# Kernel optimization log

Measured on AMD Instinct MI355X. Metric: run time of the kernel, lower is better.

The kernel has to match this reference:

```python
import jax, jax.numpy as jnp
import numpy as np

N_NODES = 50000
N_EDGES = 400000
IN_DIM = 128
HIDDEN = 128
OUT_DIM = 128
MIX = 4

def _gelu(x):
    return jax.nn.gelu(x, approximate=False)  # torch default erf-GELU

def setup_inputs() -> dict:
    key = jax.random.key(0)
    ks = jax.random.split(key, 8)
    X = jax.random.normal(ks[0], (N_NODES, IN_DIM), dtype=jnp.float32)
    edge_index = jax.random.randint(ks[1], (2, N_EDGES), 0, N_NODES, dtype=jnp.int64)
    s = lambda fan_in: 1.0 / np.sqrt(fan_in)
    W1 = jax.random.uniform(ks[2], (HIDDEN, IN_DIM), jnp.float32, -s(IN_DIM), s(IN_DIM))
    b1 = jax.random.uniform(ks[3], (HIDDEN,), jnp.float32, -s(IN_DIM), s(IN_DIM))
    WA = jax.random.uniform(ks[4], (HIDDEN, HIDDEN), jnp.float32, -s(HIDDEN), s(HIDDEN))
    WB = jax.random.uniform(ks[5], (MIX, HIDDEN), jnp.float32, -s(HIDDEN), s(HIDDEN))
    W2 = jax.random.uniform(ks[6], (OUT_DIM, 2 * HIDDEN), jnp.float32, -s(2 * HIDDEN), s(2 * HIDDEN))
    b2 = jax.random.uniform(ks[7], (OUT_DIM,), jnp.float32, -s(2 * HIDDEN), s(2 * HIDDEN))
    return {"X": X, "edge_index": edge_index, "W1": W1, "b1": b1,
            "WA": WA, "WB": WB, "W2": W2, "b2": b2}

def reference(X, edge_index, W1, b1, WA, WB, W2, b2):
    num_nodes = X.shape[0]
    # ff1 -> gelu (dropout identity in eval)
    H = _gelu(X @ W1.T + b1)                       # (N, h)
    src, dst = edge_index[0], edge_index[1]
    X_src = H[src]                                 # (E, h) gather
    # hyper target weights per edge
    W_tar = _gelu(X_src @ WA.T) @ WB.T             # (E, m)
    # per-edge outer product, scatter_add over dst
    cross = X_src[:, :, None] * W_tar[:, None, :]  # (E, h, m)
    agg = jax.ops.segment_sum(cross, dst, num_segments=num_nodes)  # (N, h, m)
    agg = _gelu(agg)
    # gather back per edge, contract mix dim
    out_edge = jnp.einsum('ehm,em->eh', agg[dst], W_tar)  # (E, h)
    # scatter_mean over dst
    ones = jnp.ones((src.shape[0],), X.dtype)
    cnt = jax.ops.segment_sum(ones, dst, num_segments=num_nodes)   # (N,)
    agg_node = jax.ops.segment_sum(out_edge, dst, num_segments=num_nodes)
    agg_node = agg_node / jnp.maximum(cnt, 1.0)[:, None]           # (N, h)
    # root connection + gelu, ff2
    feat = _gelu(jnp.concatenate([agg_node, H], axis=1))           # (N, 2h)
    out = feat @ W2.T + b2                                          # (N, out)
    return out
```

## Files before the change

kernel.cpp:

```cpp
#include <hip/hip_runtime.h>
#include <hip/hip_bf16.h>

#define NN 50000
#define NE 400000
#define NT 3125

typedef unsigned short u16;
typedef short short8 __attribute__((ext_vector_type(8)));
typedef float f32x4 __attribute__((ext_vector_type(4)));

__device__ __forceinline__ float geluf(float x){ return 0.5f*x*(1.0f+erff(x*0.70710678118654752440f)); }
__device__ __forceinline__ u16 f2bfb(float f){
  union { __hip_bfloat16 h; u16 u; } cv; cv.h = __float2bfloat16(f); return cv.u;
}
__device__ __forceinline__ float bfb2f(u16 u){ return __uint_as_float(((unsigned)u)<<16); }

__global__ __launch_bounds__(256) void k_zero(int4* __restrict__ p){
  int i = blockIdx.x*256 + threadIdx.x;
  if (i < 25024) p[i] = (int4){0,0,0,0};
}

__global__ __launch_bounds__(256) void k_pre(const float* __restrict__ W1,
    const float* __restrict__ WA, const float* __restrict__ W2,
    u16* __restrict__ W1b, u16* __restrict__ WAb, u16* __restrict__ W2r,
    const int* __restrict__ dst, int* __restrict__ deg)
{
  if (blockIdx.x < 32){
    int i4 = (blockIdx.x*256 + threadIdx.x) * 4;
    const float* srcp; u16* dstp; int off;
    if (i4 < 16384){ srcp = W1; dstp = W1b; off = i4; }
    else { srcp = WA; dstp = WAb; off = i4 - 16384; }
    float4 v = *(const float4*)(srcp + off);
    ushort4 o;
    o.x = f2bfb(v.x); o.y = f2bfb(v.y); o.z = f2bfb(v.z); o.w = f2bfb(v.w);
    *(ushort4*)(dstp + off) = o;
  } else if (blockIdx.x < 48){
    int t0 = (blockIdx.x - 32)*2048 + threadIdx.x*8;
    int lane = (t0 >> 3) & 63;
    int kk   = (t0 >> 9) & 7;
    int nb   = t0 >> 12;
    int src  = (nb*16 + (lane & 15))*256 + kk*32 + (lane >> 4)*8;
    float4 v0 = *(const float4*)(W2 + src);
    float4 v1 = *(const float4*)(W2 + src + 4);
    ushort4 o0, o1;
    o0.x = f2bfb(v0.x); o0.y = f2bfb(v0.y); o0.z = f2bfb(v0.z); o0.w = f2bfb(v0.w);
    o1.x = f2bfb(v1.x); o1.y = f2bfb(v1.y); o1.z = f2bfb(v1.z); o1.w = f2bfb(v1.w);
    *(ushort4*)(W2r + t0)     = o0;
    *(ushort4*)(W2r + t0 + 4) = o1;
  } else {
    int e = (blockIdx.x - 48)*256 + threadIdx.x;
    if (e < NE) atomicAdd(&deg[dst[e]], 1);
  }
}

__global__ __launch_bounds__(512) void k_ff1n(const float* __restrict__ X,
    const u16* __restrict__ W1b, const float* __restrict__ b1,
    const u16* __restrict__ WAb, const float* __restrict__ WB,
    u16* __restrict__ Hb, float* __restrict__ T)
{
  extern __shared__ u16 smem[];
  u16* w1s = smem;
  u16* was = smem + 17408;
  const int LDW = 136;
  for (int idx8 = threadIdx.x*8; idx8 < 128*128; idx8 += 512*8){
    int c = idx8 >> 7, k = idx8 & 127;
    *(short8*)&w1s[c*LDW + k] = *(const short8*)(W1b + idx8);
    *(short8*)&was[c*LDW + k] = *(const short8*)(WAb + idx8);
  }
  __syncthreads();
  const int lane = threadIdx.x & 63;
  const int wave = threadIdx.x >> 6;
  const int lrow = lane & 15;
  const int kgrp = lane >> 4;
  u16* hls = smem + 34816 + wave*(16*LDW);
  float4 b1v[8];
  #pragma unroll
  for (int nb = 0; nb < 8; nb++) b1v[nb] = *(const float4*)(b1 + nb*16 + kgrp*4);
  float wbv[4][8];
  #pragma unroll
  for (int m = 0; m < 4; m++)
    #pragma unroll
    for (int nb = 0; nb < 8; nb++)
      wbv[m][nb] = WB[m*128 + nb*16 + lrow];
  for (int tile = blockIdx.x*8 + wave; tile < NT; tile += gridDim.x*8){
    const float* xr = X + (size_t)(tile*16 + lrow)*128 + kgrp*8;
    f32x4 acc[8];
    #pragma unroll
    for (int nb = 0; nb < 8; nb++) acc[nb] = (f32x4){0.f,0.f,0.f,0.f};
    #pragma unroll
    for (int kk = 0; kk < 4; kk++){
      float4 xa = *(const float4*)(xr + kk*32);
      float4 xb = *(const float4*)(xr + kk*32 + 4);
      union { short8 v; u16 u[8]; } af;
      af.u[0]=f2bfb(xa.x); af.u[1]=f2bfb(xa.y); af.u[2]=f2bfb(xa.z); af.u[3]=f2bfb(xa.w);
      af.u[4]=f2bfb(xb.x); af.u[5]=f2bfb(xb.y); af.u[6]=f2bfb(xb.z); af.u[7]=f2bfb(xb.w);
      #pragma unroll
      for (int nb = 0; nb < 8; nb++){
        short8 bf = *(const short8*)&w1s[(nb*16 + lrow)*LDW + kk*32 + kgrp*8];
        acc[nb] = __builtin_amdgcn_mfma_f32_16x16x32_bf16(bf, af.v, acc[nb], 0, 0, 0);
      }
    }
    const size_t rb = (size_t)(tile*16 + lrow)*128 + kgrp*4;
    #pragma unroll
    for (int nb = 0; nb < 8; nb++){
      ushort4 hp;
      #pragma unroll
      for (int r = 0; r < 4; r++)
        ((u16*)&hp)[r] = f2bfb(geluf(acc[nb][r] + b1v[nb][r]));
      *(ushort4*)(Hb + rb + nb*16) = hp;
      *(ushort4*)&hls[lrow*LDW + nb*16 + kgrp*4] = hp;
    }
    f32x4 acc2[8];
    #pragma unroll
    for (int nb = 0; nb < 8; nb++) acc2[nb] = (f32x4){0.f,0.f,0.f,0.f};
    #pragma unroll
    for (int kk = 0; kk < 4; kk++){
      short8 af = *(const short8*)&hls[lrow*LDW + kk*32 + kgrp*8];
      #pragma unroll
      for (int nb = 0; nb < 8; nb++){
        short8 bf = *(const short8*)&was[(nb*16 + lrow)*LDW + kk*32 + kgrp*8];
        acc2[nb] = __builtin_amdgcn_mfma_f32_16x16x32_bf16(af, bf, acc2[nb], 0, 0, 0);
      }
    }
    float part[4][4];
    #pragma unroll
    for (int r = 0; r < 4; r++)
      #pragma unroll
      for (int m = 0; m < 4; m++) part[r][m] = 0.f;
    #pragma unroll
    for (int nb = 0; nb < 8; nb++){
      float g0 = geluf(acc2[nb][0]), g1 = geluf(acc2[nb][1]);
      float g2 = geluf(acc2[nb][2]), g3 = geluf(acc2[nb][3]);
      #pragma unroll
      for (int m = 0; m < 4; m++){
        float w = wbv[m][nb];
        part[0][m] += g0*w; part[1][m] += g1*w;
        part[2][m] += g2*w; part[3][m] += g3*w;
      }
    }
    #pragma unroll
    for (int s = 1; s < 16; s <<= 1)
      #pragma unroll
      for (int r = 0; r < 4; r++)
        #pragma unroll
        for (int m = 0; m < 4; m++)
          part[r][m] += __shfl_xor(part[r][m], s, 64);
    if (lrow == 0){
      #pragma unroll
      for (int r = 0; r < 4; r++){
        f32x4 tv = { part[r][0], part[r][1], part[r][2], part[r][3] };
        *(f32x4*)&T[(size_t)(tile*16 + kgrp*4 + r)*4] = tv;
      }
    }
  }
}

__global__ __launch_bounds__(1024) void k_scan(const int* __restrict__ deg, int* __restrict__ offs){
  __shared__ int wsum[16];
  __shared__ int sbase_s;
  const int tid = threadIdx.x, lane = tid & 63, wave = tid >> 6;
  if (tid == 0) sbase_s = 0;
  __syncthreads();
  for (int base = 0; base < NN; base += 4096){
    int i0 = base + tid*4;
    int v0=0,v1=0,v2=0,v3=0;
    if (i0+3 < NN){ int4 v = *(const int4*)(deg+i0); v0=v.x;v1=v.y;v2=v.z;v3=v.w; }
    else {
      if (i0   < NN) v0 = deg[i0];
      if (i0+1 < NN) v1 = deg[i0+1];
      if (i0+2 < NN) v2 = deg[i0+2];
    }
    int own = v0+v1+v2+v3;
    int inc = own;
    #pragma unroll
    for (int s=1;s<64;s<<=1){ int t = __shfl_up(inc, s, 64); if (lane >= s) inc += t; }
    if (lane == 63) wsum[wave] = inc;
    __syncthreads();
    if (wave == 0 && lane < 16){
      int w = wsum[lane];
      #pragma unroll
      for (int s=1;s<16;s<<=1){ int t = __shfl_up(w, s, 64); if (lane >= s) w += t; }
      wsum[lane] = w;
    }
    __syncthreads();
    int sbase = sbase_s;
    int wbase = sbase + (wave ? wsum[wave-1] : 0);
    int excl = wbase + inc - own;
    if (i0   < NN) offs[i0]   = excl;
    if (i0+1 < NN) offs[i0+1] = excl + v0;
    if (i0+2 < NN) offs[i0+2] = excl + v0+v1;
    if (i0+3 < NN) offs[i0+3] = excl + v0+v1+v2;
    __syncthreads();
    if (tid == 0) sbase_s = sbase + wsum[15];
    __syncthreads();
  }
  if (tid == 0) offs[NN] = sbase_s;
}

__global__ void k_fill(const int* __restrict__ src, const int* __restrict__ dst,
                       const int* __restrict__ offs, int* __restrict__ cur,
                       int* __restrict__ slist){
  int e = blockIdx.x*256 + threadIdx.x;
  if (e < NE){
    int d = dst[e];
    int p = atomicAdd(&cur[d], 1);
    slist[offs[d] + p] = src[e];
  }
}

__global__ __launch_bounds__(256) void k_agg(const u16* __restrict__ Hb,
    const float* __restrict__ T, const int* __restrict__ offs,
    const int* __restrict__ slist, u16* __restrict__ GAb)
{
  const int lane = threadIdx.x & 63;
  const int wave = threadIdx.x >> 6;
  const int vo = lane*2;
  for (int v = blockIdx.x*4 + wave; v < NN; v += gridDim.x*4){
    const int e0 = __builtin_amdgcn_readfirstlane(offs[v]);
    const int e1 = __builtin_amdgcn_readfirstlane(offs[v+1]);
    float ax0=0, ax1=0, ax2=0, ax3=0;
    float ay0=0, ay1=0, ay2=0, ay3=0;
    float s0=0, s1=0, s2=0, s3=0;
    int idx = e0;
    for (; idx + 8 <= e1; idx += 8){
      unsigned pk[8]; float4 tt[8];
      #pragma unroll
      for (int u = 0; u < 8; u++){
        int sn = slist[idx+u];
        pk[u] = *(const unsigned*)(Hb + (size_t)sn*128 + vo);
        tt[u] = *(const float4*)(T + (size_t)sn*4);
      }
      #pragma unroll
      for (int u = 0; u < 8; u++){
        float hx = bfb2f((u16)(pk[u] & 0xffffu));
        float hy = bfb2f((u16)(pk[u] >> 16));
        ax0 += hx*tt[u].x; ax1 += hx*tt[u].y; ax2 += hx*tt[u].z; ax3 += hx*tt[u].w;
        ay0 += hy*tt[u].x; ay1 += hy*tt[u].y; ay2 += hy*tt[u].z; ay3 += hy*tt[u].w;
        s0 += tt[u].x; s1 += tt[u].y; s2 += tt[u].z; s3 += tt[u].w;
      }
    }
    for (; idx + 4 <= e1; idx += 4){
      unsigned pk[4]; float4 tt[4];
      #pragma unroll
      for (int u = 0; u < 4; u++){
        int sn = slist[idx+u];
        pk[u] = *(const unsigned*)(Hb + (size_t)sn*128 + vo);
        tt[u] = *(const float4*)(T + (size_t)sn*4);
      }
      #pragma unroll
      for (int u = 0; u < 4; u++){
        float hx = bfb2f((u16)(pk[u] & 0xffffu));
        float hy = bfb2f((u16)(pk[u] >> 16));
        ax0 += hx*tt[u].x; ax1 += hx*tt[u].y; ax2 += hx*tt[u].z; ax3 += hx*tt[u].w;
        ay0 += hy*tt[u].x; ay1 += hy*tt[u].y; ay2 += hy*tt[u].z; ay3 += hy*tt[u].w;
        s0 += tt[u].x; s1 += tt[u].y; s2 += tt[u].z; s3 += tt[u].w;
      }
    }
    for (; idx < e1; idx++){
      int sn = slist[idx];
      unsigned pk = *(const unsigned*)(Hb + (size_t)sn*128 + vo);
      float hx = bfb2f((u16)(pk & 0xffffu));
      float hy = bfb2f((u16)(pk >> 16));
      float4 wt = *(const float4*)(T + (size_t)sn*4);
      ax0 += hx*wt.x; ax1 += hx*wt.y; ax2 += hx*wt.z; ax3 += hx*wt.w;
      ay0 += hy*wt.x; ay1 += hy*wt.y; ay2 += hy*wt.z; ay3 += hy*wt.w;
      s0 += wt.x; s1 += wt.y; s2 += wt.z; s3 += wt.w;
    }
    float inv = 1.0f / fmaxf((float)(e1 - e0), 1.0f);
    float ox = geluf(ax0)*s0 + geluf(ax1)*s1 + geluf(ax2)*s2 + geluf(ax3)*s3;
    float oy = geluf(ay0)*s0 + geluf(ay1)*s1 + geluf(ay2)*s2 + geluf(ay3)*s3;
    ushort2 res;
    res.x = f2bfb(geluf(ox * inv));
    res.y = f2bfb(geluf(oy * inv));
    *(ushort2*)(GAb + (size_t)v*128 + vo) = res;
  }
}

__global__ __launch_bounds__(256, 2) void k_ff2(const u16* __restrict__ GAb,
    const u16* __restrict__ Hb, const u16* __restrict__ W2r,
    const float* __restrict__ b2, float* __restrict__ out)
{
  const int lane = threadIdx.x & 63;
  const int wave = threadIdx.x >> 6;
  const int lrow = lane & 15;
  const int kgrp = lane >> 4;
  const int tile = blockIdx.x*4 + wave;
  if (tile >= NT) return;
  const int row = tile*16 + lrow;
  short8 a[8];
  {
    const u16* ga = GAb + (size_t)row*128 + kgrp*8;
    const u16* hb = Hb  + (size_t)row*128 + kgrp*8;
    #pragma unroll
    for (int kk = 0; kk < 4; kk++){
      a[kk]   = *(const short8*)(ga + kk*32);
      a[4+kk] = *(const short8*)(hb + kk*32);
    }
    #pragma unroll
    for (int kk = 4; kk < 8; kk++){
      union { short8 v; u16 u[8]; } g;
      #pragma unroll
      for (int j = 0; j < 8; j++)
        g.u[j] = f2bfb(geluf(bfb2f(((const u16*)&a[kk])[j])));
      a[kk] = g.v;
    }
  }
  f32x4 acc[8];
  #pragma unroll
  for (int nb = 0; nb < 8; nb++) acc[nb] = (f32x4){0.f,0.f,0.f,0.f};
  const u16* wbase = W2r + lane*8;
  #pragma unroll
  for (int kk = 0; kk < 8; kk++){
    #pragma unroll
    for (int nb = 0; nb < 8; nb++){
      short8 bf = *(const short8*)(wbase + (size_t)(nb*8 + kk)*512);
      acc[nb] = __builtin_amdgcn_mfma_f32_16x16x32_bf16(bf, a[kk], acc[nb], 0, 0, 0);
    }
  }
  float* orp = out + (size_t)row*128 + kgrp*4;
  #pragma unroll
  for (int nb = 0; nb < 8; nb++){
    float4 bv = *(const float4*)(b2 + nb*16 + kgrp*4);
    f32x4 o;
    o[0] = acc[nb][0] + bv.x;
    o[1] = acc[nb][1] + bv.y;
    o[2] = acc[nb][2] + bv.z;
    o[3] = acc[nb][3] + bv.w;
    *(f32x4*)(orp + nb*16) = o;
  }
}

extern "C" void kernel_launch(void* const* d_in, const int* in_sizes, int n_in,
                              void* d_out, int out_size, void* d_ws, size_t ws_size,
                              hipStream_t stream)
{
  (void)in_sizes; (void)n_in; (void)out_size; (void)ws_size;
  const float* X  = (const float*)d_in[0];
  const int*   ei = (const int*)d_in[1];
  const float* W1 = (const float*)d_in[2];
  const float* b1 = (const float*)d_in[3];
  const float* WA = (const float*)d_in[4];
  const float* WB = (const float*)d_in[5];
  const float* W2 = (const float*)d_in[6];
  const float* b2 = (const float*)d_in[7];
  float* out = (float*)d_out;
  const int* src = ei;
  const int* dst = ei + NE;

  char* p = (char*)d_ws;
  u16*   Hb   = (u16*)(p);
  u16*   GAb  = (u16*)(p + 12800000);
  float* T    = (float*)(p + 25600000);
  int*   deg  = (int*)(p + 26400000);
  int*   cur  = (int*)(p + 26600192);
  int*   offs = (int*)(p + 26800384);
  int*   slist= (int*)(p + 27000832);
  u16*   W1b  = (u16*)(p + 28600832);
  u16*   WAb  = (u16*)(p + 28633600);
  u16*   W2r  = (u16*)(p + 28666368);

  (void)hipFuncSetAttribute((const void*)k_ff1n, hipFuncAttributeMaxDynamicSharedMemorySize, 104448);

  k_zero<<<98, 256, 0, stream>>>((int4*)deg);
  k_pre <<<48 + (NE+255)/256, 256, 0, stream>>>(W1, WA, W2, W1b, WAb, W2r, dst, deg);
  k_ff1n<<<391, 512, 104448, stream>>>(X, W1b, b1, WAb, WB, Hb, T);
  k_scan<<<1, 1024, 0, stream>>>(deg, offs);
  k_fill<<<(NE+255)/256, 256, 0, stream>>>(src, dst, offs, cur, slist);
  k_agg <<<2048, 256, 0, stream>>>(Hb, T, offs, slist, GAb);
  k_ff2 <<<(NT+3)/4, 256, 0, stream>>>(GAb, Hb, W2r, b2, out);
}
```

Before: 144.1 us.

## Pre-swizzle W1/WA into MFMA fragment layout and split ff2 across column halves

The weight-prep kernel now writes W1 and WA in a per-lane MFMA fragment order, so k_ff1n reads B fragments straight from global memory/L2 instead of staging 64KB of weights in LDS. This removes the LDS fill and block sync and cuts dynamic shared memory from 104KB to 34KB, which should allow more resident blocks per CU. k_ff2 now assigns each wave half of the output columns for a 16-row tile, doubling the wave count to raise parallelism. The cost is that the A fragments and GELU of the H half are computed twice, and the fragment loads in k_ff1n now go through global/cache traffic.

```diff
diff --git a/kernel.cpp b/kernel.cpp
--- a/kernel.cpp
+++ b/kernel.cpp
@@ -22,20 +22,26 @@
 
 __global__ __launch_bounds__(256) void k_pre(const float* __restrict__ W1,
     const float* __restrict__ WA, const float* __restrict__ W2,
-    u16* __restrict__ W1b, u16* __restrict__ WAb, u16* __restrict__ W2r,
+    u16* __restrict__ W1r, u16* __restrict__ WAr, u16* __restrict__ W2r,
     const int* __restrict__ dst, int* __restrict__ deg)
 {
-  if (blockIdx.x < 32){
-    int i4 = (blockIdx.x*256 + threadIdx.x) * 4;
-    const float* srcp; u16* dstp; int off;
-    if (i4 < 16384){ srcp = W1; dstp = W1b; off = i4; }
-    else { srcp = WA; dstp = WAb; off = i4 - 16384; }
-    float4 v = *(const float4*)(srcp + off);
-    ushort4 o;
-    o.x = f2bfb(v.x); o.y = f2bfb(v.y); o.z = f2bfb(v.z); o.w = f2bfb(v.w);
-    *(ushort4*)(dstp + off) = o;
-  } else if (blockIdx.x < 48){
-    int t0 = (blockIdx.x - 32)*2048 + threadIdx.x*8;
+  if (blockIdx.x < 16){
+    const float* srcp = (blockIdx.x < 8) ? W1 : WA;
+    u16* dstp = (blockIdx.x < 8) ? W1r : WAr;
+    int t0 = ((blockIdx.x & 7)*256 + threadIdx.x)*8;
+    int lane = (t0 >> 3) & 63;
+    int kk   = (t0 >> 9) & 3;
+    int nb   = t0 >> 11;
+    int src  = (nb*16 + (lane & 15))*128 + kk*32 + (lane >> 4)*8;
+    float4 v0 = *(const float4*)(srcp + src);
+    float4 v1 = *(const float4*)(srcp + src + 4);
+    ushort4 o0, o1;
+    o0.x = f2bfb(v0.x); o0.y = f2bfb(v0.y); o0.z = f2bfb(v0.z); o0.w = f2bfb(v0.w);
+    o1.x = f2bfb(v1.x); o1.y = f2bfb(v1.y); o1.z = f2bfb(v1.z); o1.w = f2bfb(v1.w);
+    *(ushort4*)(dstp + t0)     = o0;
+    *(ushort4*)(dstp + t0 + 4) = o1;
+  } else if (blockIdx.x < 32){
+    int t0 = ((blockIdx.x - 16)*256 + threadIdx.x)*8;
     int lane = (t0 >> 3) & 63;
     int kk   = (t0 >> 9) & 7;
     int nb   = t0 >> 12;
@@ -48,31 +54,23 @@
     *(ushort4*)(W2r + t0)     = o0;
     *(ushort4*)(W2r + t0 + 4) = o1;
   } else {
-    int e = (blockIdx.x - 48)*256 + threadIdx.x;
+    int e = (blockIdx.x - 32)*256 + threadIdx.x;
     if (e < NE) atomicAdd(&deg[dst[e]], 1);
   }
 }
 
 __global__ __launch_bounds__(512) void k_ff1n(const float* __restrict__ X,
-    const u16* __restrict__ W1b, const float* __restrict__ b1,
-    const u16* __restrict__ WAb, const float* __restrict__ WB,
+    const u16* __restrict__ W1r, const float* __restrict__ b1,
+    const u16* __restrict__ WAr, const float* __restrict__ WB,
     u16* __restrict__ Hb, float* __restrict__ T)
 {
   extern __shared__ u16 smem[];
-  u16* w1s = smem;
-  u16* was = smem + 17408;
   const int LDW = 136;
-  for (int idx8 = threadIdx.x*8; idx8 < 128*128; idx8 += 512*8){
-    int c = idx8 >> 7, k = idx8 & 127;
-    *(short8*)&w1s[c*LDW + k] = *(const short8*)(W1b + idx8);
-    *(short8*)&was[c*LDW + k] = *(const short8*)(WAb + idx8);
-  }
-  __syncthreads();
   const int lane = threadIdx.x & 63;
   const int wave = threadIdx.x >> 6;
   const int lrow = lane & 15;
   const int kgrp = lane >> 4;
-  u16* hls = smem + 34816 + wave*(16*LDW);
+  u16* hls = smem + wave*(16*LDW);
   float4 b1v[8];
   #pragma unroll
   for (int nb = 0; nb < 8; nb++) b1v[nb] = *(const float4*)(b1 + nb*16 + kgrp*4);
@@ -82,6 +80,8 @@
     #pragma unroll
     for (int nb = 0; nb < 8; nb++)
       wbv[m][nb] = WB[m*128 + nb*16 + lrow];
+  const u16* w1base = W1r + lane*8;
+  const u16* wabase = WAr + lane*8;
   for (int tile = blockIdx.x*8 + wave; tile < NT; tile += gridDim.x*8){
     const float* xr = X + (size_t)(tile*16 + lrow)*128 + kgrp*8;
     f32x4 acc[8];
@@ -96,7 +96,7 @@
       af.u[4]=f2bfb(xb.x); af.u[5]=f2bfb(xb.y); af.u[6]=f2bfb(xb.z); af.u[7]=f2bfb(xb.w);
       #pragma unroll
       for (int nb = 0; nb < 8; nb++){
-        short8 bf = *(const short8*)&w1s[(nb*16 + lrow)*LDW + kk*32 + kgrp*8];
+        short8 bf = *(const short8*)(w1base + (nb*4 + kk)*512);
         acc[nb] = __builtin_amdgcn_mfma_f32_16x16x32_bf16(bf, af.v, acc[nb], 0, 0, 0);
       }
     }
@@ -118,7 +118,7 @@
       short8 af = *(const short8*)&hls[lrow*LDW + kk*32 + kgrp*8];
       #pragma unroll
       for (int nb = 0; nb < 8; nb++){
-        short8 bf = *(const short8*)&was[(nb*16 + lrow)*LDW + kk*32 + kgrp*8];
+        short8 bf = *(const short8*)(wabase + (nb*4 + kk)*512);
         acc2[nb] = __builtin_amdgcn_mfma_f32_16x16x32_bf16(af, bf, acc2[nb], 0, 0, 0);
       }
     }
@@ -284,7 +284,9 @@
   const int wave = threadIdx.x >> 6;
   const int lrow = lane & 15;
   const int kgrp = lane >> 4;
-  const int tile = blockIdx.x*4 + wave;
+  const int widx = blockIdx.x*4 + wave;
+  const int tile = widx >> 1;
+  const int nbh  = (widx & 1)*4;
   if (tile >= NT) return;
   const int row = tile*16 + lrow;
   short8 a[8];
@@ -305,28 +307,28 @@
       a[kk] = g.v;
     }
   }
-  f32x4 acc[8];
-  #pragma unroll
-  for (int nb = 0; nb < 8; nb++) acc[nb] = (f32x4){0.f,0.f,0.f,0.f};
+  f32x4 acc[4];
+  #pragma unroll
+  for (int q = 0; q < 4; q++) acc[q] = (f32x4){0.f,0.f,0.f,0.f};
   const u16* wbase = W2r + lane*8;
   #pragma unroll
   for (int kk = 0; kk < 8; kk++){
     #pragma unroll
-    for (int nb = 0; nb < 8; nb++){
-      short8 bf = *(const short8*)(wbase + (size_t)(nb*8 + kk)*512);
-      acc[nb] = __builtin_amdgcn_mfma_f32_16x16x32_bf16(bf, a[kk], acc[nb], 0, 0, 0);
-    }
-  }
-  float* orp = out + (size_t)row*128 + kgrp*4;
-  #pragma unroll
-  for (int nb = 0; nb < 8; nb++){
-    float4 bv = *(const float4*)(b2 + nb*16 + kgrp*4);
+    for (int q = 0; q < 4; q++){
+      short8 bf = *(const short8*)(wbase + (size_t)((nbh + q)*8 + kk)*512);
+      acc[q] = __builtin_amdgcn_mfma_f32_16x16x32_bf16(bf, a[kk], acc[q], 0, 0, 0);
+    }
+  }
+  float* orp = out + (size_t)row*128 + nbh*16 + kgrp*4;
+  #pragma unroll
+  for (int q = 0; q < 4; q++){
+    float4 bv = *(const float4*)(b2 + (nbh + q)*16 + kgrp*4);
     f32x4 o;
-    o[0] = acc[nb][0] + bv.x;
-    o[1] = acc[nb][1] + bv.y;
-    o[2] = acc[nb][2] + bv.z;
-    o[3] = acc[nb][3] + bv.w;
-    *(f32x4*)(orp + nb*16) = o;
+    o[0] = acc[q][0] + bv.x;
+    o[1] = acc[q][1] + bv.y;
+    o[2] = acc[q][2] + bv.z;
+    o[3] = acc[q][3] + bv.w;
+    *(f32x4*)(orp + q*16) = o;
   }
 }
 
@@ -355,17 +357,15 @@
   int*   cur  = (int*)(p + 26600192);
   int*   offs = (int*)(p + 26800384);
   int*   slist= (int*)(p + 27000832);
-  u16*   W1b  = (u16*)(p + 28600832);
-  u16*   WAb  = (u16*)(p + 28633600);
+  u16*   W1r  = (u16*)(p + 28600832);
+  u16*   WAr  = (u16*)(p + 28633600);
   u16*   W2r  = (u16*)(p + 28666368);
 
-  (void)hipFuncSetAttribute((const void*)k_ff1n, hipFuncAttributeMaxDynamicSharedMemorySize, 104448);
-
   k_zero<<<98, 256, 0, stream>>>((int4*)deg);
-  k_pre <<<48 + (NE+255)/256, 256, 0, stream>>>(W1, WA, W2, W1b, WAb, W2r, dst, deg);
-  k_ff1n<<<391, 512, 104448, stream>>>(X, W1b, b1, WAb, WB, Hb, T);
+  k_pre <<<32 + (NE+255)/256, 256, 0, stream>>>(W1, WA, W2, W1r, WAr, W2r, dst, deg);
+  k_ff1n<<<391, 512, 34816, stream>>>(X, W1r, b1, WAr, WB, Hb, T);
   k_scan<<<1, 1024, 0, stream>>>(deg, offs);
   k_fill<<<(NE+255)/256, 256, 0, stream>>>(src, dst, offs, cur, slist);
   k_agg <<<2048, 256, 0, stream>>>(Hb, T, offs, slist, GAb);
-  k_ff2 <<<(NT+3)/4, 256, 0, stream>>>(GAb, Hb, W2r, b2, out);
-}
+  k_ff2 <<<(2*NT+3)/4, 256, 0, stream>>>(GAb, Hb, W2r, b2, out);
+}
```

Result: slower. 197.5 us (+37.1%).
